# Kernel tuning notes

Measured on AMD Instinct MI355X. Metric: run time of the kernel, lower is better.

Reference implementation:

```python
import jax, jax.numpy as jnp
import numpy as np

EMBED_DIM = 512
Q_DIM = 64
V_DIM = 64
WINDOW_SIZE = 128
B, N = 2, 4096


def setup_inputs() -> dict:
    key = jax.random.key(0)
    ks = jax.random.split(key, 7)
    s = 1.0 / np.sqrt(EMBED_DIM)
    u = lambda k, shape: jax.random.uniform(k, shape, jnp.float32, -s, s)
    return {
        "x": jax.random.normal(ks[0], (B, N, EMBED_DIM), jnp.float32),
        "Wq": u(ks[1], (EMBED_DIM, Q_DIM)),
        "bq": u(ks[2], (Q_DIM,)),
        "Wk": u(ks[3], (EMBED_DIM, Q_DIM)),
        "bk": u(ks[4], (Q_DIM,)),
        "Wv": u(ks[5], (EMBED_DIM, V_DIM)),
        "bv": u(ks[6], (V_DIM,)),
    }


def reference(x, Wq, bq, Wk, bk, Wv, bv):
    b, n, _ = x.shape
    w = WINDOW_SIZE // 2
    Q = x @ Wq + bq  # (b, n, Qd)
    K = x @ Wk + bk  # (b, n, Qd)
    V = x @ Wv + bv  # (b, n, Vd)

    diags = jnp.arange(-w, w + 1)            # (nd,) offsets di
    nd = diags.shape[0]
    # Gather K[i + di] via padded K; invalid positions masked to 0 afterwards.
    Kpad = jnp.pad(K, ((0, 0), (w, w), (0, 0)))
    j = jnp.arange(n)[:, None] + diags[None, :]          # (n, nd) = i + di
    Kg = Kpad[:, j + w, :]                               # (b, n, nd, Qd)
    scores = jnp.einsum('bnd,bnod->bno', Q, Kg)          # (b, n, nd)
    valid = (j >= 0) & (j < n)
    scores = jnp.where(valid[None], scores, 0.0)

    # Faithful to original: diagonal dot products are scattered into the FIRST
    # nd columns of a dense (b, n, n) matrix (rest zeros), softmax over the
    # full n columns, then dense matmul with V.
    columns = jnp.zeros((b, n, n), dtype=x.dtype).at[:, :, :nd].set(scores)
    attn = jax.nn.softmax(columns, axis=2)               # (b, n, n)
    return attn @ V                                      # (b, n, Vd)
```

## Files before the change

### kernel.cpp

```cpp
#include <hip/hip_runtime.h>

typedef short short8 __attribute__((ext_vector_type(8)));
typedef float f32x4 __attribute__((ext_vector_type(4)));

#define NN 4096
#define NE 512
#define HD 64
#define KROWS 4288
#define KOFF  64

__device__ __forceinline__ unsigned short bf_trunc(float f) {
    union { float f; unsigned u; } c; c.f = f;
    return (unsigned short)(c.u >> 16);
}
__device__ __forceinline__ void bf_split(float f, unsigned short& hi, unsigned short& lo) {
    union { float f; unsigned u; } c; c.f = f;
    unsigned uh = c.u & 0xFFFF0000u;
    hi = (unsigned short)(uh >> 16);
    union { float f; unsigned u; } d; d.u = uh;
    lo = bf_trunc(f - d.f);
}

#define MFMA16(a, b, c) __builtin_amdgcn_mfma_f32_16x16x32_bf16((a), (b), (c), 0, 0, 0)

__global__ __launch_bounds__(256) void wprep_kernel(
    const float* __restrict__ Wq, const float* __restrict__ Wk,
    const float* __restrict__ Wv,
    unsigned short* __restrict__ Wfhi, unsigned short* __restrict__ Wflo,
    unsigned short* __restrict__ Khi, unsigned short* __restrict__ Klo,
    float* __restrict__ Vs)
{
    const int gtid = blockIdx.x * 256 + threadIdx.x;
    {
        const int L = gtid & 63;
        const int nt = (gtid >> 6) % 12;
        const int kt = gtid / 768;
        const int n = nt * 16 + (L & 15);
        const int kbase = kt * 32 + (L >> 4) * 8;
        const float* src; int col;
        if (n < 64)       { src = Wq; col = n; }
        else if (n < 128) { src = Wk; col = n - 64; }
        else              { src = Wv; col = n - 128; }
        short8 sh, sl;
#pragma unroll
        for (int j = 0; j < 8; ++j) {
            unsigned short h, l;
            bf_split(src[(size_t)(kbase + j) * HD + col], h, l);
            sh[j] = (short)h; sl[j] = (short)l;
        }
        *(short8*)(Wfhi + (size_t)gtid * 8) = sh;
        *(short8*)(Wflo + (size_t)gtid * 8) = sl;
    }
    if (gtid < 6144) {
        const int p = gtid >> 3, o = gtid & 7;
        const int b = p / 192, q = p - b * 192;
        const size_t row = (size_t)b * KROWS + (q < 64 ? q : 4096 + q);
        const short8 z = {0, 0, 0, 0, 0, 0, 0, 0};
        *(short8*)(Khi + row * HD + o * 8) = z;
        *(short8*)(Klo + row * HD + o * 8) = z;
    }
    if (gtid < 128) Vs[gtid] = 0.f;
}

__global__ __launch_bounds__(512) void proj_kernel(
    const float* __restrict__ x,
    const unsigned short* __restrict__ Wfhi, const unsigned short* __restrict__ Wflo,
    const float* __restrict__ bq, const float* __restrict__ bk,
    const float* __restrict__ bv,
    unsigned short* __restrict__ Qhi, unsigned short* __restrict__ Qlo,
    unsigned short* __restrict__ Khi, unsigned short* __restrict__ Klo,
    float* __restrict__ V129, float* __restrict__ Vs)
{
    __shared__ float vred[8][64];
    const int tid = threadIdx.x;
    const int L = tid & 63;
    const int w = tid >> 6;
    const int rt = w & 1, cg3 = w >> 1;
    const int m = L & 15, kg = L >> 4;
    const int r0 = blockIdx.x * 32;
    const int rowbase = r0 + rt * 16;

    const float* xp_base = x + (size_t)(rowbase + m) * NE + kg * 8;
    const unsigned short* wfh_base = Wfhi + (size_t)(cg3 * 3) * 512 + L * 8;
    const unsigned short* wfl_base = Wflo + (size_t)(cg3 * 3) * 512 + L * 8;

    f32x4 acc[3];
#pragma unroll
    for (int t = 0; t < 3; ++t) acc[t] = (f32x4){0.f, 0.f, 0.f, 0.f};

    float4 xa0 = *(const float4*)(xp_base);
    float4 xa1 = *(const float4*)(xp_base + 4);
    short8 wh0 = *(const short8*)(wfh_base + 0 * 512);
    short8 wh1 = *(const short8*)(wfh_base + 1 * 512);
    short8 wh2 = *(const short8*)(wfh_base + 2 * 512);
    short8 wl0 = *(const short8*)(wfl_base + 0 * 512);
    short8 wl1 = *(const short8*)(wfl_base + 1 * 512);
    short8 wl2 = *(const short8*)(wfl_base + 2 * 512);

    for (int kt = 0; kt < 16; ++kt) {
        const int ktn = (kt < 15) ? kt + 1 : 15;
        const float* xn = xp_base + ktn * 32;
        const float4 xb0 = *(const float4*)(xn);
        const float4 xb1 = *(const float4*)(xn + 4);
        const unsigned short* wnh = wfh_base + (size_t)ktn * 6144;
        const unsigned short* wnl = wfl_base + (size_t)ktn * 6144;
        const short8 nh0 = *(const short8*)(wnh);
        const short8 nh1 = *(const short8*)(wnh + 512);
        const short8 nh2 = *(const short8*)(wnh + 1024);
        const short8 nl0 = *(const short8*)(wnl);
        const short8 nl1 = *(const short8*)(wnl + 512);
        const short8 nl2 = *(const short8*)(wnl + 1024);

        const float xv[8] = {xa0.x, xa0.y, xa0.z, xa0.w,
                             xa1.x, xa1.y, xa1.z, xa1.w};
        short8 ahi, alo;
#pragma unroll
        for (int j = 0; j < 8; ++j) {
            unsigned short h, l; bf_split(xv[j], h, l);
            ahi[j] = (short)h; alo[j] = (short)l;
        }
        acc[0] = MFMA16(ahi, wh0, acc[0]);
        acc[0] = MFMA16(alo, wh0, acc[0]);
        acc[0] = MFMA16(ahi, wl0, acc[0]);
        acc[1] = MFMA16(ahi, wh1, acc[1]);
        acc[1] = MFMA16(alo, wh1, acc[1]);
        acc[1] = MFMA16(ahi, wl1, acc[1]);
        acc[2] = MFMA16(ahi, wh2, acc[2]);
        acc[2] = MFMA16(alo, wh2, acc[2]);
        acc[2] = MFMA16(ahi, wl2, acc[2]);

        xa0 = xb0; xa1 = xb1;
        wh0 = nh0; wh1 = nh1; wh2 = nh2;
        wl0 = nl0; wl1 = nl1; wl2 = nl2;
    }

    const int b = r0 >> 12;
#pragma unroll
    for (int t = 0; t < 3; ++t) {
        const int nt = cg3 * 3 + t;
        const int cg = nt * 16 + m;
        const float bias = (cg < 64) ? bq[cg] : (cg < 128) ? bk[cg - 64] : bv[cg - 128];
        float vsump = 0.f;
#pragma unroll
        for (int r = 0; r < 4; ++r) {
            const int gr = rowbase + kg * 4 + r;
            const float val = acc[t][r] + bias;
            if (cg < 64) {
                unsigned short h, l; bf_split(val, h, l);
                Qhi[(size_t)gr * HD + cg] = h;
                Qlo[(size_t)gr * HD + cg] = l;
            } else if (cg < 128) {
                const int d = cg - 64, n = gr & 4095;
                const size_t idx = ((size_t)b * KROWS + KOFF + n) * HD + d;
                unsigned short h, l; bf_split(val, h, l);
                Khi[idx] = h; Klo[idx] = l;
            } else {
                const int d = cg - 128, n = gr & 4095;
                vsump += val;
                if (n < 129) V129[((size_t)b * 129 + n) * HD + d] = val;
            }
        }
        if (cg >= 128) vred[rt * 4 + kg][cg - 128] = vsump;
    }
    __syncthreads();
    if (tid < 64) {
        float s = 0.f;
#pragma unroll
        for (int g = 0; g < 8; ++g) s += vred[g][tid];
        atomicAdd(&Vs[b * HD + tid], s);
    }
}

__global__ __launch_bounds__(256) void vprep_kernel(
    const float* __restrict__ V129,
    unsigned short* __restrict__ Vfhi, unsigned short* __restrict__ Vflo)
{
    const int tid = blockIdx.x * 256 + threadIdx.x;
    if (tid >= 3200) return;
    const int L = tid & 63;
    const int nt = (tid >> 6) % 5;
    const int jt = (tid / 320) % 5;
    const int b  = tid / 1600;
    const int n  = nt * 16 + (L & 15);
    const int jb = jt * 32 + (L >> 4) * 8;
    short8 sh, sl;
#pragma unroll
    for (int jj = 0; jj < 8; ++jj) {
        const int j = jb + jj;
        float val = 0.f;
        if (j < 129) {
            if (n < 64)       val = V129[((size_t)b * 129 + j) * HD + n];
            else if (n == 64) val = 1.0f;
        }
        unsigned short h, l; bf_split(val, h, l);
        sh[jj] = (short)h; sl[jj] = (short)l;
    }
    *(short8*)(Vfhi + (size_t)tid * 8) = sh;
    *(short8*)(Vflo + (size_t)tid * 8) = sl;
}

__global__ __launch_bounds__(256) void attn_kernel(
    const unsigned short* __restrict__ Qhi, const unsigned short* __restrict__ Qlo,
    const unsigned short* __restrict__ Khi, const unsigned short* __restrict__ Klo,
    const unsigned short* __restrict__ Vfhi, const unsigned short* __restrict__ Vflo,
    const float* __restrict__ Vs, float* __restrict__ out)
{
    __shared__ __align__(16) unsigned short wt_hi[16 * 168];
    __shared__ __align__(16) unsigned short wt_lo[16 * 168];
    __shared__ float den_lds[16];

    const int tid = threadIdx.x;
    const int L = tid & 63;
    const int w = tid >> 6;
    const int m = L & 15, kg = L >> 4;
    const int b = blockIdx.x >> 8;
    const int n0 = (blockIdx.x & 255) * 16;

    const unsigned short* qp  = Qhi + ((size_t)(b * NN + n0 + m)) * HD + kg * 8;
    const unsigned short* qp2 = Qlo + ((size_t)(b * NN + n0 + m)) * HD + kg * 8;
    const short8 qhi0 = *(const short8*)(qp);
    const short8 qhi1 = *(const short8*)(qp + 32);
    const short8 qlo0 = *(const short8*)(qp2);
    const short8 qlo1 = *(const short8*)(qp2 + 32);

    int kts[3]; int nkt;
    if (w == 3) { kts[0] = 3; kts[1] = 7; kts[2] = 8; nkt = 3; }
    else        { kts[0] = w; kts[1] = w + 4; kts[2] = 0; nkt = 2; }

    const unsigned short* KB  = Khi + (size_t)b * KROWS * HD;
    const unsigned short* KB2 = Klo + (size_t)b * KROWS * HD;
    short8 kh0[3], kh1[3], kl0[3], kl1[3];
#pragma unroll
    for (int i = 0; i < 3; ++i) {
        if (i < nkt) {
            const size_t krow = (size_t)(n0 + kts[i] * 16 + m);
            const unsigned short* kp  = KB  + krow * HD + kg * 8;
            const unsigned short* kp2 = KB2 + krow * HD + kg * 8;
            kh0[i] = *(const short8*)(kp);
            kh1[i] = *(const short8*)(kp + 32);
            kl0[i] = *(const short8*)(kp2);
            kl1[i] = *(const short8*)(kp2 + 32);
        }
    }

    short8 vhi[5], vlo[5], vh4[5];
#pragma unroll
    for (int jt = 0; jt < 5; ++jt) {
        const size_t fo = ((size_t)((b * 25 + jt * 5 + w) * 64 + L)) * 8;
        vhi[jt] = *(const short8*)(Vfhi + fo);
        vlo[jt] = *(const short8*)(Vflo + fo);
    }
    if (w == 0) {
#pragma unroll
        for (int jt = 0; jt < 5; ++jt) {
            const size_t fo4 = ((size_t)((b * 25 + jt * 5 + 4) * 64 + L)) * 8;
            vh4[jt] = *(const short8*)(Vfhi + fo4);
        }
    }

    for (int i = tid; i < (16 * 168) / 2; i += 256) {
        ((int*)wt_hi)[i] = 0;
        ((int*)wt_lo)[i] = 0;
    }
    __syncthreads();

#pragma unroll
    for (int i = 0; i < 3; ++i) {
        if (i < nkt) {
            f32x4 acc = (f32x4){0.f, 0.f, 0.f, 0.f};
            acc = MFMA16(qhi0, kh0[i], acc);
            acc = MFMA16(qhi1, kh1[i], acc);
            acc = MFMA16(qlo0, kh0[i], acc);
            acc = MFMA16(qlo1, kh1[i], acc);
            acc = MFMA16(qhi0, kl0[i], acc);
            acc = MFMA16(qhi1, kl1[i], acc);
            const int l = kts[i] * 16 + m;
#pragma unroll
            for (int r = 0; r < 4; ++r) {
                const int q = kg * 4 + r;
                const int j = l - q;
                if (j >= 0 && j < 129) {
                    const float wv = __expf(acc[r]) - 1.0f;
                    unsigned short h, lo2; bf_split(wv, h, lo2);
                    wt_hi[q * 168 + j] = h;
                    wt_lo[q * 168 + j] = lo2;
                }
            }
        }
    }
    __syncthreads();

    f32x4 oacc = (f32x4){0.f, 0.f, 0.f, 0.f};
    f32x4 dacc = (f32x4){0.f, 0.f, 0.f, 0.f};
#pragma unroll
    for (int jt = 0; jt < 5; ++jt) {
        const short8 whi = *(const short8*)(wt_hi + m * 168 + jt * 32 + kg * 8);
        const short8 wlo = *(const short8*)(wt_lo + m * 168 + jt * 32 + kg * 8);
        oacc = MFMA16(whi, vhi[jt], oacc);
        oacc = MFMA16(wlo, vhi[jt], oacc);
        oacc = MFMA16(whi, vlo[jt], oacc);
        if (w == 0) {
            dacc = MFMA16(whi, vh4[jt], dacc);
            dacc = MFMA16(wlo, vh4[jt], dacc);
        }
    }
    if (w == 0 && m == 0) {
#pragma unroll
        for (int r = 0; r < 4; ++r) den_lds[kg * 4 + r] = dacc[r];
    }
    __syncthreads();

    {
        const float vs = Vs[b * HD + w * 16 + m];
#pragma unroll
        for (int r = 0; r < 4; ++r) {
            const int q = kg * 4 + r;
            const float val = (vs + oacc[r]) / (4096.f + den_lds[q]);
            out[((size_t)(b * NN + n0 + q)) * HD + w * 16 + m] = val;
        }
    }
}

extern "C" void kernel_launch(void* const* d_in, const int* in_sizes, int n_in,
                              void* d_out, int out_size, void* d_ws, size_t ws_size,
                              hipStream_t stream)
{
    const float* x  = (const float*)d_in[0];
    const float* Wq = (const float*)d_in[1];
    const float* bq = (const float*)d_in[2];
    const float* Wk = (const float*)d_in[3];
    const float* bk = (const float*)d_in[4];
    const float* Wv = (const float*)d_in[5];
    const float* bv = (const float*)d_in[6];
    float* out = (float*)d_out;

    char* ws = (char*)d_ws;
    float*          Vs   = (float*)(ws + 0);
    unsigned short* Khi  = (unsigned short*)(ws + 512);
    unsigned short* Klo  = (unsigned short*)(ws + 1098240);
    unsigned short* Qhi  = (unsigned short*)(ws + 2195968);
    unsigned short* Qlo  = (unsigned short*)(ws + 3244544);
    float*          V129 = (float*)(ws + 4293120);
    unsigned short* Wfhi = (unsigned short*)(ws + 4359168);
    unsigned short* Wflo = (unsigned short*)(ws + 4555776);
    unsigned short* Vfhi = (unsigned short*)(ws + 4752384);
    unsigned short* Vflo = (unsigned short*)(ws + 4803584);

    wprep_kernel<<<48, 256, 0, stream>>>(Wq, Wk, Wv, Wfhi, Wflo, Khi, Klo, Vs);
    proj_kernel<<<256, 512, 0, stream>>>(x, Wfhi, Wflo, bq, bk, bv,
                                         Qhi, Qlo, Khi, Klo, V129, Vs);
    vprep_kernel<<<13, 256, 0, stream>>>(V129, Vfhi, Vflo);
    attn_kernel<<<512, 256, 0, stream>>>(Qhi, Qlo, Khi, Klo, Vfhi, Vflo, Vs, out);
}
```

Baseline: 102.3 us.

## Fuse four kernels into one cooperative kernel with grid-wide syncs

Replaces the four separate launches (weight prep, projection, V prep, attention) with a single cooperative kernel of 256 blocks of 512 threads, separated by grid.sync barriers. Each attention block now handles two 16-row query groups using two LDS buffers. The aim is to remove the per-launch overhead and the gaps between dependent kernels. In exchange it pays for three grid-wide barriers, depends on cooperative launch support, and limits the attention stage to 256 blocks.

Measured after the change: 185.1 us. 81.0% more time.

```diff
diff --git a/kernel.cpp b/kernel.cpp
--- a/kernel.cpp
+++ b/kernel.cpp
@@ -1,4 +1,7 @@
 #include <hip/hip_runtime.h>
+#include <hip/hip_cooperative_groups.h>
+
+namespace cg = cooperative_groups;
 
 typedef short short8 __attribute__((ext_vector_type(8)));
 typedef float f32x4 __attribute__((ext_vector_type(4)));
@@ -23,300 +26,300 @@
 
 #define MFMA16(a, b, c) __builtin_amdgcn_mfma_f32_16x16x32_bf16((a), (b), (c), 0, 0, 0)
 
-__global__ __launch_bounds__(256) void wprep_kernel(
-    const float* __restrict__ Wq, const float* __restrict__ Wk,
-    const float* __restrict__ Wv,
+__global__ __launch_bounds__(512) void fused_kernel(
+    const float* __restrict__ x,
+    const float* __restrict__ Wq, const float* __restrict__ bq,
+    const float* __restrict__ Wk, const float* __restrict__ bk,
+    const float* __restrict__ Wv, const float* __restrict__ bv,
     unsigned short* __restrict__ Wfhi, unsigned short* __restrict__ Wflo,
-    unsigned short* __restrict__ Khi, unsigned short* __restrict__ Klo,
-    float* __restrict__ Vs)
-{
-    const int gtid = blockIdx.x * 256 + threadIdx.x;
-    {
-        const int L = gtid & 63;
-        const int nt = (gtid >> 6) % 12;
-        const int kt = gtid / 768;
-        const int n = nt * 16 + (L & 15);
-        const int kbase = kt * 32 + (L >> 4) * 8;
-        const float* src; int col;
-        if (n < 64)       { src = Wq; col = n; }
-        else if (n < 128) { src = Wk; col = n - 64; }
-        else              { src = Wv; col = n - 128; }
-        short8 sh, sl;
-#pragma unroll
-        for (int j = 0; j < 8; ++j) {
-            unsigned short h, l;
-            bf_split(src[(size_t)(kbase + j) * HD + col], h, l);
-            sh[j] = (short)h; sl[j] = (short)l;
-        }
-        *(short8*)(Wfhi + (size_t)gtid * 8) = sh;
-        *(short8*)(Wflo + (size_t)gtid * 8) = sl;
-    }
-    if (gtid < 6144) {
-        const int p = gtid >> 3, o = gtid & 7;
-        const int b = p / 192, q = p - b * 192;
-        const size_t row = (size_t)b * KROWS + (q < 64 ? q : 4096 + q);
-        const short8 z = {0, 0, 0, 0, 0, 0, 0, 0};
-        *(short8*)(Khi + row * HD + o * 8) = z;
-        *(short8*)(Klo + row * HD + o * 8) = z;
-    }
-    if (gtid < 128) Vs[gtid] = 0.f;
-}
-
-__global__ __launch_bounds__(512) void proj_kernel(
-    const float* __restrict__ x,
-    const unsigned short* __restrict__ Wfhi, const unsigned short* __restrict__ Wflo,
-    const float* __restrict__ bq, const float* __restrict__ bk,
-    const float* __restrict__ bv,
     unsigned short* __restrict__ Qhi, unsigned short* __restrict__ Qlo,
     unsigned short* __restrict__ Khi, unsigned short* __restrict__ Klo,
-    float* __restrict__ V129, float* __restrict__ Vs)
+    float* __restrict__ V129,
+    unsigned short* __restrict__ Vfhi, unsigned short* __restrict__ Vflo,
+    float* __restrict__ Vs, float* __restrict__ out)
 {
-    __shared__ float vred[8][64];
-    const int tid = threadIdx.x;
-    const int L = tid & 63;
-    const int w = tid >> 6;
-    const int rt = w & 1, cg3 = w >> 1;
-    const int m = L & 15, kg = L >> 4;
-    const int r0 = blockIdx.x * 32;
-    const int rowbase = r0 + rt * 16;
-
-    const float* xp_base = x + (size_t)(rowbase + m) * NE + kg * 8;
-    const unsigned short* wfh_base = Wfhi + (size_t)(cg3 * 3) * 512 + L * 8;
-    const unsigned short* wfl_base = Wflo + (size_t)(cg3 * 3) * 512 + L * 8;
-
-    f32x4 acc[3];
-#pragma unroll
-    for (int t = 0; t < 3; ++t) acc[t] = (f32x4){0.f, 0.f, 0.f, 0.f};
-
-    float4 xa0 = *(const float4*)(xp_base);
-    float4 xa1 = *(const float4*)(xp_base + 4);
-    short8 wh0 = *(const short8*)(wfh_base + 0 * 512);
-    short8 wh1 = *(const short8*)(wfh_base + 1 * 512);
-    short8 wh2 = *(const short8*)(wfh_base + 2 * 512);
-    short8 wl0 = *(const short8*)(wfl_base + 0 * 512);
-    short8 wl1 = *(const short8*)(wfl_base + 1 * 512);
-    short8 wl2 = *(const short8*)(wfl_base + 2 * 512);
-
-    for (int kt = 0; kt < 16; ++kt) {
-        const int ktn = (kt < 15) ? kt + 1 : 15;
-        const float* xn = xp_base + ktn * 32;
-        const float4 xb0 = *(const float4*)(xn);
-        const float4 xb1 = *(const float4*)(xn + 4);
-        const unsigned short* wnh = wfh_base + (size_t)ktn * 6144;
-        const unsigned short* wnl = wfl_base + (size_t)ktn * 6144;
-        const short8 nh0 = *(const short8*)(wnh);
-        const short8 nh1 = *(const short8*)(wnh + 512);
-        const short8 nh2 = *(const short8*)(wnh + 1024);
-        const short8 nl0 = *(const short8*)(wnl);
-        const short8 nl1 = *(const short8*)(wnl + 512);
-        const short8 nl2 = *(const short8*)(wnl + 1024);
-
-        const float xv[8] = {xa0.x, xa0.y, xa0.z, xa0.w,
-                             xa1.x, xa1.y, xa1.z, xa1.w};
-        short8 ahi, alo;
-#pragma unroll
-        for (int j = 0; j < 8; ++j) {
-            unsigned short h, l; bf_split(xv[j], h, l);
-            ahi[j] = (short)h; alo[j] = (short)l;
-        }
-        acc[0] = MFMA16(ahi, wh0, acc[0]);
-        acc[0] = MFMA16(alo, wh0, acc[0]);
-        acc[0] = MFMA16(ahi, wl0, acc[0]);
-        acc[1] = MFMA16(ahi, wh1, acc[1]);
-        acc[1] = MFMA16(alo, wh1, acc[1]);
-        acc[1] = MFMA16(ahi, wl1, acc[1]);
-        acc[2] = MFMA16(ahi, wh2, acc[2]);
-        acc[2] = MFMA16(alo, wh2, acc[2]);
-        acc[2] = MFMA16(ahi, wl2, acc[2]);
-
-        xa0 = xb0; xa1 = xb1;
-        wh0 = nh0; wh1 = nh1; wh2 = nh2;
-        wl0 = nl0; wl1 = nl1; wl2 = nl2;
-    }
-
-    const int b = r0 >> 12;
-#pragma unroll
-    for (int t = 0; t < 3; ++t) {
-        const int nt = cg3 * 3 + t;
-        const int cg = nt * 16 + m;
-        const float bias = (cg < 64) ? bq[cg] : (cg < 128) ? bk[cg - 64] : bv[cg - 128];
-        float vsump = 0.f;
-#pragma unroll
-        for (int r = 0; r < 4; ++r) {
-            const int gr = rowbase + kg * 4 + r;
-            const float val = acc[t][r] + bias;
-            if (cg < 64) {
-                unsigned short h, l; bf_split(val, h, l);
-                Qhi[(size_t)gr * HD + cg] = h;
-                Qlo[(size_t)gr * HD + cg] = l;
-            } else if (cg < 128) {
-                const int d = cg - 64, n = gr & 4095;
-                const size_t idx = ((size_t)b * KROWS + KOFF + n) * HD + d;
-                unsigned short h, l; bf_split(val, h, l);
-                Khi[idx] = h; Klo[idx] = l;
-            } else {
-                const int d = cg - 128, n = gr & 4095;
-                vsump += val;
-                if (n < 129) V129[((size_t)b * 129 + n) * HD + d] = val;
-            }
-        }
-        if (cg >= 128) vred[rt * 4 + kg][cg - 128] = vsump;
-    }
-    __syncthreads();
-    if (tid < 64) {
-        float s = 0.f;
-#pragma unroll
-        for (int g = 0; g < 8; ++g) s += vred[g][tid];
-        atomicAdd(&Vs[b * HD + tid], s);
-    }
-}
-
-__global__ __launch_bounds__(256) void vprep_kernel(
-    const float* __restrict__ V129,
-    unsigned short* __restrict__ Vfhi, unsigned short* __restrict__ Vflo)
-{
-    const int tid = blockIdx.x * 256 + threadIdx.x;
-    if (tid >= 3200) return;
-    const int L = tid & 63;
-    const int nt = (tid >> 6) % 5;
-    const int jt = (tid / 320) % 5;
-    const int b  = tid / 1600;
-    const int n  = nt * 16 + (L & 15);
-    const int jb = jt * 32 + (L >> 4) * 8;
-    short8 sh, sl;
-#pragma unroll
-    for (int jj = 0; jj < 8; ++jj) {
-        const int j = jb + jj;
-        float val = 0.f;
-        if (j < 129) {
-            if (n < 64)       val = V129[((size_t)b * 129 + j) * HD + n];
-            else if (n == 64) val = 1.0f;
-        }
-        unsigned short h, l; bf_split(val, h, l);
-        sh[jj] = (short)h; sl[jj] = (short)l;
-    }
-    *(short8*)(Vfhi + (size_t)tid * 8) = sh;
-    *(short8*)(Vflo + (size_t)tid * 8) = sl;
-}
-
-__global__ __launch_bounds__(256) void attn_kernel(
-    const unsigned short* __restrict__ Qhi, const unsigned short* __restrict__ Qlo,
-    const unsigned short* __restrict__ Khi, const unsigned short* __restrict__ Klo,
-    const unsigned short* __restrict__ Vfhi, const unsigned short* __restrict__ Vflo,
-    const float* __restrict__ Vs, float* __restrict__ out)
-{
-    __shared__ __align__(16) unsigned short wt_hi[16 * 168];
-    __shared__ __align__(16) unsigned short wt_lo[16 * 168];
-    __shared__ float den_lds[16];
-
+    cg::grid_group grid = cg::this_grid();
+    const int blk = blockIdx.x;
     const int tid = threadIdx.x;
     const int L = tid & 63;
     const int w = tid >> 6;
     const int m = L & 15, kg = L >> 4;
-    const int b = blockIdx.x >> 8;
-    const int n0 = (blockIdx.x & 255) * 16;
-
-    const unsigned short* qp  = Qhi + ((size_t)(b * NN + n0 + m)) * HD + kg * 8;
-    const unsigned short* qp2 = Qlo + ((size_t)(b * NN + n0 + m)) * HD + kg * 8;
-    const short8 qhi0 = *(const short8*)(qp);
-    const short8 qhi1 = *(const short8*)(qp + 32);
-    const short8 qlo0 = *(const short8*)(qp2);
-    const short8 qlo1 = *(const short8*)(qp2 + 32);
-
-    int kts[3]; int nkt;
-    if (w == 3) { kts[0] = 3; kts[1] = 7; kts[2] = 8; nkt = 3; }
-    else        { kts[0] = w; kts[1] = w + 4; kts[2] = 0; nkt = 2; }
-
-    const unsigned short* KB  = Khi + (size_t)b * KROWS * HD;
-    const unsigned short* KB2 = Klo + (size_t)b * KROWS * HD;
-    short8 kh0[3], kh1[3], kl0[3], kl1[3];
-#pragma unroll
-    for (int i = 0; i < 3; ++i) {
-        if (i < nkt) {
-            const size_t krow = (size_t)(n0 + kts[i] * 16 + m);
-            const unsigned short* kp  = KB  + krow * HD + kg * 8;
-            const unsigned short* kp2 = KB2 + krow * HD + kg * 8;
-            kh0[i] = *(const short8*)(kp);
-            kh1[i] = *(const short8*)(kp + 32);
-            kl0[i] = *(const short8*)(kp2);
-            kl1[i] = *(const short8*)(kp2 + 32);
-        }
+
+    __shared__ float vred[8][64];
+    __shared__ __align__(16) unsigned short wt_hi[2][16 * 168];
+    __shared__ __align__(16) unsigned short wt_lo[2][16 * 168];
+    __shared__ float den_lds[2][16];
+
+    {
+        const int gtid = blk * 512 + tid;
+        if (gtid < 12288) {
+            const int nt = (gtid >> 6) % 12;
+            const int kt = gtid / 768;
+            const int n = nt * 16 + m;
+            const int kbase = kt * 32 + kg * 8;
+            const float* src; int col;
+            if (n < 64)       { src = Wq; col = n; }
+            else if (n < 128) { src = Wk; col = n - 64; }
+            else              { src = Wv; col = n - 128; }
+            short8 sh, sl;
+#pragma unroll
+            for (int j = 0; j < 8; ++j) {
+                unsigned short h, l;
+                bf_split(src[(size_t)(kbase + j) * HD + col], h, l);
+                sh[j] = (short)h; sl[j] = (short)l;
+            }
+            *(short8*)(Wfhi + (size_t)gtid * 8) = sh;
+            *(short8*)(Wflo + (size_t)gtid * 8) = sl;
+        }
+        if (gtid < 6144) {
+            const int p = gtid >> 3, o = gtid & 7;
+            const int b = p / 192, q = p - b * 192;
+            const size_t row = (size_t)b * KROWS + (q < 64 ? q : 4096 + q);
+            const short8 z = {0, 0, 0, 0, 0, 0, 0, 0};
+            *(short8*)(Khi + row * HD + o * 8) = z;
+            *(short8*)(Klo + row * HD + o * 8) = z;
+        }
+        if (gtid < 128) Vs[gtid] = 0.f;
     }
-
-    short8 vhi[5], vlo[5], vh4[5];
-#pragma unroll
-    for (int jt = 0; jt < 5; ++jt) {
-        const size_t fo = ((size_t)((b * 25 + jt * 5 + w) * 64 + L)) * 8;
-        vhi[jt] = *(const short8*)(Vfhi + fo);
-        vlo[jt] = *(const short8*)(Vflo + fo);
+    grid.sync();
+
+    {
+        const int rt = w & 1, cg3 = w >> 1;
+        const int r0 = blk * 32;
+        const int rowbase = r0 + rt * 16;
+
+        const float* xp_base = x + (size_t)(rowbase + m) * NE + kg * 8;
+        const unsigned short* wfh_base = Wfhi + (size_t)(cg3 * 3) * 512 + L * 8;
+        const unsigned short* wfl_base = Wflo + (size_t)(cg3 * 3) * 512 + L * 8;
+
+        f32x4 acc[3];
+#pragma unroll
+        for (int t = 0; t < 3; ++t) acc[t] = (f32x4){0.f, 0.f, 0.f, 0.f};
+
+        float4 xa0 = *(const float4*)(xp_base);
+        float4 xa1 = *(const float4*)(xp_base + 4);
+        short8 wh0 = *(const short8*)(wfh_base + 0 * 512);
+        short8 wh1 = *(const short8*)(wfh_base + 1 * 512);
+        short8 wh2 = *(const short8*)(wfh_base + 2 * 512);
+        short8 wl0 = *(const short8*)(wfl_base + 0 * 512);
+        short8 wl1 = *(const short8*)(wfl_base + 1 * 512);
+        short8 wl2 = *(const short8*)(wfl_base + 2 * 512);
+
+#pragma unroll 2
+        for (int kt = 0; kt < 16; ++kt) {
+            const int ktn = (kt < 15) ? kt + 1 : 15;
+            const float* xn = xp_base + ktn * 32;
+            const float4 xb0 = *(const float4*)(xn);
+            const float4 xb1 = *(const float4*)(xn + 4);
+            const unsigned short* wnh = wfh_base + (size_t)ktn * 6144;
+            const unsigned short* wnl = wfl_base + (size_t)ktn * 6144;
+            const short8 nh0 = *(const short8*)(wnh);
+            const short8 nh1 = *(const short8*)(wnh + 512);
+            const short8 nh2 = *(const short8*)(wnh + 1024);
+            const short8 nl0 = *(const short8*)(wnl);
+            const short8 nl1 = *(const short8*)(wnl + 512);
+            const short8 nl2 = *(const short8*)(wnl + 1024);
+
+            const float xv[8] = {xa0.x, xa0.y, xa0.z, xa0.w,
+                                 xa1.x, xa1.y, xa1.z, xa1.w};
+            short8 ahi, alo;
+#pragma unroll
+            for (int j = 0; j < 8; ++j) {
+                unsigned short h, l; bf_split(xv[j], h, l);
+                ahi[j] = (short)h; alo[j] = (short)l;
+            }
+            acc[0] = MFMA16(ahi, wh0, acc[0]);
+            acc[0] = MFMA16(alo, wh0, acc[0]);
+            acc[0] = MFMA16(ahi, wl0, acc[0]);
+            acc[1] = MFMA16(ahi, wh1, acc[1]);
+            acc[1] = MFMA16(alo, wh1, acc[1]);
+            acc[1] = MFMA16(ahi, wl1, acc[1]);
+            acc[2] = MFMA16(ahi, wh2, acc[2]);
+            acc[2] = MFMA16(alo, wh2, acc[2]);
+            acc[2] = MFMA16(ahi, wl2, acc[2]);
+
+            xa0 = xb0; xa1 = xb1;
+            wh0 = nh0; wh1 = nh1; wh2 = nh2;
+            wl0 = nl0; wl1 = nl1; wl2 = nl2;
+        }
+
+        const int b = r0 >> 12;
+#pragma unroll
+        for (int t = 0; t < 3; ++t) {
+            const int nt = cg3 * 3 + t;
+            const int cgc = nt * 16 + m;
+            const float bias = (cgc < 64) ? bq[cgc]
+                             : (cgc < 128) ? bk[cgc - 64] : bv[cgc - 128];
+            float vsump = 0.f;
+#pragma unroll
+            for (int r = 0; r < 4; ++r) {
+                const int gr = rowbase + kg * 4 + r;
+                const float val = acc[t][r] + bias;
+                if (cgc < 64) {
+                    unsigned short h, l; bf_split(val, h, l);
+                    Qhi[(size_t)gr * HD + cgc] = h;
+                    Qlo[(size_t)gr * HD + cgc] = l;
+                } else if (cgc < 128) {
+                    const int d = cgc - 64, n = gr & 4095;
+                    const size_t idx = ((size_t)b * KROWS + KOFF + n) * HD + d;
+                    unsigned short h, l; bf_split(val, h, l);
+                    Khi[idx] = h; Klo[idx] = l;
+                } else {
+                    const int d = cgc - 128, n = gr & 4095;
+                    vsump += val;
+                    if (n < 129) V129[((size_t)b * 129 + n) * HD + d] = val;
+                }
+            }
+            if (cgc >= 128) vred[rt * 4 + kg][cgc - 128] = vsump;
+        }
+        __syncthreads();
+        if (tid < 64) {
+            float s = 0.f;
+#pragma unroll
+            for (int g = 0; g < 8; ++g) s += vred[g][tid];
+            atomicAdd(&Vs[b * HD + tid], s);
+        }
     }
-    if (w == 0) {
+    grid.sync();
+
+    {
+        const int gtid = blk * 512 + tid;
+        if (gtid < 3200) {
+            const int nt = (gtid >> 6) % 5;
+            const int jt = (gtid / 320) % 5;
+            const int b  = gtid / 1600;
+            const int n  = nt * 16 + m;
+            const int jb = jt * 32 + kg * 8;
+            short8 sh, sl;
+#pragma unroll
+            for (int jj = 0; jj < 8; ++jj) {
+                const int j = jb + jj;
+                float val = 0.f;
+                if (j < 129) {
+                    if (n < 64)       val = V129[((size_t)b * 129 + j) * HD + n];
+                    else if (n == 64) val = 1.0f;
+                }
+                unsigned short h, l; bf_split(val, h, l);
+                sh[jj] = (short)h; sl[jj] = (short)l;
+            }
+            *(short8*)(Vfhi + (size_t)gtid * 8) = sh;
+            *(short8*)(Vflo + (size_t)gtid * 8) = sl;
+        }
+    }
+    grid.sync();
+
+    {
+        const int g  = w >> 2;
+        const int wv = w & 3;
+        const int vblk = blk * 2 + g;
+        const int b  = vblk >> 8;
+        const int n0 = (vblk & 255) * 16;
+
+        const unsigned short* qp  = Qhi + ((size_t)(b * NN + n0 + m)) * HD + kg * 8;
+        const unsigned short* qp2 = Qlo + ((size_t)(b * NN + n0 + m)) * HD + kg * 8;
+        const short8 qhi0 = *(const short8*)(qp);
+        const short8 qhi1 = *(const short8*)(qp + 32);
+        const short8 qlo0 = *(const short8*)(qp2);
+        const short8 qlo1 = *(const short8*)(qp2 + 32);
+
+        int kts[3]; int nkt;
+        if (wv == 3) { kts[0] = 3; kts[1] = 7; kts[2] = 8; nkt = 3; }
+        else         { kts[0] = wv; kts[1] = wv + 4; kts[2] = 0; nkt = 2; }
+
+        const unsigned short* KB  = Khi + (size_t)b * KROWS * HD;
+        const unsigned short* KB2 = Klo + (size_t)b * KROWS * HD;
+        short8 kh0[3], kh1[3], kl0[3], kl1[3];
+#pragma unroll
+        for (int i = 0; i < 3; ++i) {
+            if (i < nkt) {
+                const size_t krow = (size_t)(n0 + kts[i] * 16 + m);
+                const unsigned short* kp  = KB  + krow * HD + kg * 8;
+                const unsigned short* kp2 = KB2 + krow * HD + kg * 8;
+                kh0[i] = *(const short8*)(kp);
+                kh1[i] = *(const short8*)(kp + 32);
+                kl0[i] = *(const short8*)(kp2);
+                kl1[i] = *(const short8*)(kp2 + 32);
+            }
+        }
+
+        short8 vhi[5], vlo[5], vh4[5];
 #pragma unroll
         for (int jt = 0; jt < 5; ++jt) {
-            const size_t fo4 = ((size_t)((b * 25 + jt * 5 + 4) * 64 + L)) * 8;
-            vh4[jt] = *(const short8*)(Vfhi + fo4);
-        }
-    }
-
-    for (int i = tid; i < (16 * 168) / 2; i += 256) {
-        ((int*)wt_hi)[i] = 0;
-        ((int*)wt_lo)[i] = 0;
-    }
-    __syncthreads();
-
-#pragma unroll
-    for (int i = 0; i < 3; ++i) {
-        if (i < nkt) {
-            f32x4 acc = (f32x4){0.f, 0.f, 0.f, 0.f};
-            acc = MFMA16(qhi0, kh0[i], acc);
-            acc = MFMA16(qhi1, kh1[i], acc);
-            acc = MFMA16(qlo0, kh0[i], acc);
-            acc = MFMA16(qlo1, kh1[i], acc);
-            acc = MFMA16(qhi0, kl0[i], acc);
-            acc = MFMA16(qhi1, kl1[i], acc);
-            const int l = kts[i] * 16 + m;
+            const size_t fo = ((size_t)((b * 25 + jt * 5 + wv) * 64 + L)) * 8;
+            vhi[jt] = *(const short8*)(Vfhi + fo);
+            vlo[jt] = *(const short8*)(Vflo + fo);
+        }
+        if (wv == 0) {
+#pragma unroll
+            for (int jt = 0; jt < 5; ++jt) {
+                const size_t fo4 = ((size_t)((b * 25 + jt * 5 + 4) * 64 + L)) * 8;
+                vh4[jt] = *(const short8*)(Vfhi + fo4);
+            }
+        }
+
+        {
+            const int lt = (wv << 6) | L;
+            for (int i = lt; i < (16 * 168) / 2; i += 256) {
+                ((int*)wt_hi[g])[i] = 0;
+                ((int*)wt_lo[g])[i] = 0;
+            }
+        }
+        __syncthreads();
+
+#pragma unroll
+        for (int i = 0; i < 3; ++i) {
+            if (i < nkt) {
+                f32x4 acc = (f32x4){0.f, 0.f, 0.f, 0.f};
+                acc = MFMA16(qhi0, kh0[i], acc);
+                acc = MFMA16(qhi1, kh1[i], acc);
+                acc = MFMA16(qlo0, kh0[i], acc);
+                acc = MFMA16(qlo1, kh1[i], acc);
+                acc = MFMA16(qhi0, kl0[i], acc);
+                acc = MFMA16(qhi1, kl1[i], acc);
+                const int l = kts[i] * 16 + m;
+#pragma unroll
+                for (int r = 0; r < 4; ++r) {
+                    const int q = kg * 4 + r;
+                    const int j = l - q;
+                    if (j >= 0 && j < 129) {
+                        const float wval = __expf(acc[r]) - 1.0f;
+                        unsigned short h, lo2; bf_split(wval, h, lo2);
+                        wt_hi[g][q * 168 + j] = h;
+                        wt_lo[g][q * 168 + j] = lo2;
+                    }
+                }
+            }
+        }
+        __syncthreads();
+
+        f32x4 oacc = (f32x4){0.f, 0.f, 0.f, 0.f};
+        f32x4 dacc = (f32x4){0.f, 0.f, 0.f, 0.f};
+#pragma unroll
+        for (int jt = 0; jt < 5; ++jt) {
+            const short8 whi = *(const short8*)(wt_hi[g] + m * 168 + jt * 32 + kg * 8);
+            const short8 wlo = *(const short8*)(wt_lo[g] + m * 168 + jt * 32 + kg * 8);
+            oacc = MFMA16(whi, vhi[jt], oacc);
+            oacc = MFMA16(wlo, vhi[jt], oacc);
+            oacc = MFMA16(whi, vlo[jt], oacc);
+            if (wv == 0) {
+                dacc = MFMA16(whi, vh4[jt], dacc);
+                dacc = MFMA16(wlo, vh4[jt], dacc);
+            }
+        }
+        if (wv == 0 && m == 0) {
+#pragma unroll
+            for (int r = 0; r < 4; ++r) den_lds[g][kg * 4 + r] = dacc[r];
+        }
+        __syncthreads();
+
+        {
+            const float vs = Vs[b * HD + wv * 16 + m];
 #pragma unroll
             for (int r = 0; r < 4; ++r) {
                 const int q = kg * 4 + r;
-                const int j = l - q;
-                if (j >= 0 && j < 129) {
-                    const float wv = __expf(acc[r]) - 1.0f;
-                    unsigned short h, lo2; bf_split(wv, h, lo2);
-                    wt_hi[q * 168 + j] = h;
-                    wt_lo[q * 168 + j] = lo2;
-                }
-            }
-        }
-    }
-    __syncthreads();
-
-    f32x4 oacc = (f32x4){0.f, 0.f, 0.f, 0.f};
-    f32x4 dacc = (f32x4){0.f, 0.f, 0.f, 0.f};
-#pragma unroll
-    for (int jt = 0; jt < 5; ++jt) {
-        const short8 whi = *(const short8*)(wt_hi + m * 168 + jt * 32 + kg * 8);
-        const short8 wlo = *(const short8*)(wt_lo + m * 168 + jt * 32 + kg * 8);
-        oacc = MFMA16(whi, vhi[jt], oacc);
-        oacc = MFMA16(wlo, vhi[jt], oacc);
-        oacc = MFMA16(whi, vlo[jt], oacc);
-        if (w == 0) {
-            dacc = MFMA16(whi, vh4[jt], dacc);
-            dacc = MFMA16(wlo, vh4[jt], dacc);
-        }
-    }
-    if (w == 0 && m == 0) {
-#pragma unroll
-        for (int r = 0; r < 4; ++r) den_lds[kg * 4 + r] = dacc[r];
-    }
-    __syncthreads();
-
-    {
-        const float vs = Vs[b * HD + w * 16 + m];
-#pragma unroll
-        for (int r = 0; r < 4; ++r) {
-            const int q = kg * 4 + r;
-            const float val = (vs + oacc[r]) / (4096.f + den_lds[q]);
-            out[((size_t)(b * NN + n0 + q)) * HD + w * 16 + m] = val;
+                const float val = (vs + oacc[r]) / (4096.f + den_lds[g][q]);
+                out[((size_t)(b * NN + n0 + q)) * HD + wv * 16 + m] = val;
+            }
         }
     }
 }
@@ -346,9 +349,14 @@
     unsigned short* Vfhi = (unsigned short*)(ws + 4752384);
     unsigned short* Vflo = (unsigned short*)(ws + 4803584);
 
-    wprep_kernel<<<48, 256, 0, stream>>>(Wq, Wk, Wv, Wfhi, Wflo, Khi, Klo, Vs);
-    proj_kernel<<<256, 512, 0, stream>>>(x, Wfhi, Wflo, bq, bk, bv,
-                                         Qhi, Qlo, Khi, Klo, V129, Vs);
-    vprep_kernel<<<13, 256, 0, stream>>>(V129, Vfhi, Vflo);
-    attn_kernel<<<512, 256, 0, stream>>>(Qhi, Qlo, Khi, Klo, Vfhi, Vflo, Vs, out);
+    void* kargs[] = {
+        (void*)&x, (void*)&Wq, (void*)&bq, (void*)&Wk, (void*)&bk,
+        (void*)&Wv, (void*)&bv,
+        (void*)&Wfhi, (void*)&Wflo,
+        (void*)&Qhi, (void*)&Qlo, (void*)&Khi, (void*)&Klo,
+        (void*)&V129, (void*)&Vfhi, (void*)&Vflo,
+        (void*)&Vs, (void*)&out
+    };
+    hipLaunchCooperativeKernel(fused_kernel, dim3(256), dim3(512),
+                               kargs, 0, stream);
 }
```

## Fold V fragment prep into projection kernel and deepen load pipeline

Applied to the files above, without the earlier changes.

Removes the separate vprep kernel and its V129 intermediate. The projection kernel now writes the bf16 hi/lo V fragments straight from a shared-memory tile of V, and wprep pre-fills the constant ones-column and zero padding. The projection kernel moves to 16-row blocks of 256 threads (512 blocks, two per CU via launch bounds) with a three-stage register prefetch of x and weights. The aim is one fewer launch and no global round trip for V, at the cost of more registers for the deeper prefetch.

Result: slower. 104.6 us (+2.2%).

```diff
diff --git a/kernel.cpp b/kernel.cpp
--- a/kernel.cpp
+++ b/kernel.cpp
@@ -28,11 +28,12 @@
     const float* __restrict__ Wv,
     unsigned short* __restrict__ Wfhi, unsigned short* __restrict__ Wflo,
     unsigned short* __restrict__ Khi, unsigned short* __restrict__ Klo,
+    unsigned short* __restrict__ Vfhi, unsigned short* __restrict__ Vflo,
     float* __restrict__ Vs)
 {
     const int gtid = blockIdx.x * 256 + threadIdx.x;
+    const int L = gtid & 63;
     {
-        const int L = gtid & 63;
         const int nt = (gtid >> 6) % 12;
         const int kt = gtid / 768;
         const int n = nt * 16 + (L & 15);
@@ -59,144 +60,148 @@
         *(short8*)(Khi + row * HD + o * 8) = z;
         *(short8*)(Klo + row * HD + o * 8) = z;
     }
+    if (gtid < 3200) {
+        const int rem = gtid % 1600;
+        const int jt = rem / 320;
+        const int nt = (rem / 64) % 5;
+        short8 sh = {0, 0, 0, 0, 0, 0, 0, 0};
+        const short8 z = {0, 0, 0, 0, 0, 0, 0, 0};
+        if (nt == 4 && (L & 15) == 0) {
+#pragma unroll
+            for (int jj = 0; jj < 8; ++jj) {
+                const int j = jt * 32 + (L >> 4) * 8 + jj;
+                if (j < 129) sh[jj] = (short)0x3F80;
+            }
+        }
+        *(short8*)(Vfhi + (size_t)gtid * 8) = sh;
+        *(short8*)(Vflo + (size_t)gtid * 8) = z;
+    }
     if (gtid < 128) Vs[gtid] = 0.f;
 }
 
-__global__ __launch_bounds__(512) void proj_kernel(
+__global__ __launch_bounds__(256, 2) void proj_kernel(
     const float* __restrict__ x,
     const unsigned short* __restrict__ Wfhi, const unsigned short* __restrict__ Wflo,
     const float* __restrict__ bq, const float* __restrict__ bk,
     const float* __restrict__ bv,
     unsigned short* __restrict__ Qhi, unsigned short* __restrict__ Qlo,
     unsigned short* __restrict__ Khi, unsigned short* __restrict__ Klo,
-    float* __restrict__ V129, float* __restrict__ Vs)
+    unsigned short* __restrict__ Vfhi, unsigned short* __restrict__ Vflo,
+    float* __restrict__ Vs)
 {
-    __shared__ float vred[8][64];
+    __shared__ float V_lds[16][68];
     const int tid = threadIdx.x;
     const int L = tid & 63;
     const int w = tid >> 6;
-    const int rt = w & 1, cg3 = w >> 1;
     const int m = L & 15, kg = L >> 4;
-    const int r0 = blockIdx.x * 32;
-    const int rowbase = r0 + rt * 16;
-
-    const float* xp_base = x + (size_t)(rowbase + m) * NE + kg * 8;
-    const unsigned short* wfh_base = Wfhi + (size_t)(cg3 * 3) * 512 + L * 8;
-    const unsigned short* wfl_base = Wflo + (size_t)(cg3 * 3) * 512 + L * 8;
+    const int blk = blockIdx.x;
+    const int r0 = blk * 16;
+    const int b = blk >> 8;
+
+    const float* xp = x + (size_t)(r0 + m) * NE + kg * 8;
+    const unsigned short* wfh = Wfhi + (size_t)(w * 3) * 512 + L * 8;
+    const unsigned short* wfl = Wflo + (size_t)(w * 3) * 512 + L * 8;
 
     f32x4 acc[3];
 #pragma unroll
     for (int t = 0; t < 3; ++t) acc[t] = (f32x4){0.f, 0.f, 0.f, 0.f};
 
-    float4 xa0 = *(const float4*)(xp_base);
-    float4 xa1 = *(const float4*)(xp_base + 4);
-    short8 wh0 = *(const short8*)(wfh_base + 0 * 512);
-    short8 wh1 = *(const short8*)(wfh_base + 1 * 512);
-    short8 wh2 = *(const short8*)(wfh_base + 2 * 512);
-    short8 wl0 = *(const short8*)(wfl_base + 0 * 512);
-    short8 wl1 = *(const short8*)(wfl_base + 1 * 512);
-    short8 wl2 = *(const short8*)(wfl_base + 2 * 512);
-
+    float4 cx0[3], cx1[3];
+    short8 cwh[3][3], cwl[3][3];
+
+#pragma unroll
+    for (int p = 0; p < 2; ++p) {
+        cx0[p] = *(const float4*)(xp + p * 32);
+        cx1[p] = *(const float4*)(xp + p * 32 + 4);
+#pragma unroll
+        for (int t = 0; t < 3; ++t) {
+            cwh[p][t] = *(const short8*)(wfh + (size_t)p * 6144 + t * 512);
+            cwl[p][t] = *(const short8*)(wfl + (size_t)p * 6144 + t * 512);
+        }
+    }
+
+#pragma unroll
     for (int kt = 0; kt < 16; ++kt) {
-        const int ktn = (kt < 15) ? kt + 1 : 15;
-        const float* xn = xp_base + ktn * 32;
-        const float4 xb0 = *(const float4*)(xn);
-        const float4 xb1 = *(const float4*)(xn + 4);
-        const unsigned short* wnh = wfh_base + (size_t)ktn * 6144;
-        const unsigned short* wnl = wfl_base + (size_t)ktn * 6144;
-        const short8 nh0 = *(const short8*)(wnh);
-        const short8 nh1 = *(const short8*)(wnh + 512);
-        const short8 nh2 = *(const short8*)(wnh + 1024);
-        const short8 nl0 = *(const short8*)(wnl);
-        const short8 nl1 = *(const short8*)(wnl + 512);
-        const short8 nl2 = *(const short8*)(wnl + 1024);
-
-        const float xv[8] = {xa0.x, xa0.y, xa0.z, xa0.w,
-                             xa1.x, xa1.y, xa1.z, xa1.w};
+        const int cur = kt % 3;
+        const int nxt = (kt + 2) % 3;
+        if (kt + 2 < 16) {
+            cx0[nxt] = *(const float4*)(xp + (kt + 2) * 32);
+            cx1[nxt] = *(const float4*)(xp + (kt + 2) * 32 + 4);
+#pragma unroll
+            for (int t = 0; t < 3; ++t) {
+                cwh[nxt][t] = *(const short8*)(wfh + (size_t)(kt + 2) * 6144 + t * 512);
+                cwl[nxt][t] = *(const short8*)(wfl + (size_t)(kt + 2) * 6144 + t * 512);
+            }
+        }
+        const float xv[8] = {cx0[cur].x, cx0[cur].y, cx0[cur].z, cx0[cur].w,
+                             cx1[cur].x, cx1[cur].y, cx1[cur].z, cx1[cur].w};
         short8 ahi, alo;
 #pragma unroll
         for (int j = 0; j < 8; ++j) {
             unsigned short h, l; bf_split(xv[j], h, l);
             ahi[j] = (short)h; alo[j] = (short)l;
         }
-        acc[0] = MFMA16(ahi, wh0, acc[0]);
-        acc[0] = MFMA16(alo, wh0, acc[0]);
-        acc[0] = MFMA16(ahi, wl0, acc[0]);
-        acc[1] = MFMA16(ahi, wh1, acc[1]);
-        acc[1] = MFMA16(alo, wh1, acc[1]);
-        acc[1] = MFMA16(ahi, wl1, acc[1]);
-        acc[2] = MFMA16(ahi, wh2, acc[2]);
-        acc[2] = MFMA16(alo, wh2, acc[2]);
-        acc[2] = MFMA16(ahi, wl2, acc[2]);
-
-        xa0 = xb0; xa1 = xb1;
-        wh0 = nh0; wh1 = nh1; wh2 = nh2;
-        wl0 = nl0; wl1 = nl1; wl2 = nl2;
-    }
-
-    const int b = r0 >> 12;
+#pragma unroll
+        for (int t = 0; t < 3; ++t) {
+            acc[t] = MFMA16(ahi, cwh[cur][t], acc[t]);
+            acc[t] = MFMA16(alo, cwh[cur][t], acc[t]);
+            acc[t] = MFMA16(ahi, cwl[cur][t], acc[t]);
+        }
+    }
+
 #pragma unroll
     for (int t = 0; t < 3; ++t) {
-        const int nt = cg3 * 3 + t;
-        const int cg = nt * 16 + m;
-        const float bias = (cg < 64) ? bq[cg] : (cg < 128) ? bk[cg - 64] : bv[cg - 128];
-        float vsump = 0.f;
+        const int nt = w * 3 + t;
+        const int cgc = nt * 16 + m;
+        const float bias = (cgc < 64) ? bq[cgc]
+                         : (cgc < 128) ? bk[cgc - 64] : bv[cgc - 128];
 #pragma unroll
         for (int r = 0; r < 4; ++r) {
-            const int gr = rowbase + kg * 4 + r;
+            const int gr = r0 + kg * 4 + r;
             const float val = acc[t][r] + bias;
-            if (cg < 64) {
+            if (cgc < 64) {
                 unsigned short h, l; bf_split(val, h, l);
-                Qhi[(size_t)gr * HD + cg] = h;
-                Qlo[(size_t)gr * HD + cg] = l;
-            } else if (cg < 128) {
-                const int d = cg - 64, n = gr & 4095;
+                Qhi[(size_t)gr * HD + cgc] = h;
+                Qlo[(size_t)gr * HD + cgc] = l;
+            } else if (cgc < 128) {
+                const int d = cgc - 64, n = gr & 4095;
                 const size_t idx = ((size_t)b * KROWS + KOFF + n) * HD + d;
                 unsigned short h, l; bf_split(val, h, l);
                 Khi[idx] = h; Klo[idx] = l;
             } else {
-                const int d = cg - 128, n = gr & 4095;
-                vsump += val;
-                if (n < 129) V129[((size_t)b * 129 + n) * HD + d] = val;
-            }
-        }
-        if (cg >= 128) vred[rt * 4 + kg][cg - 128] = vsump;
+                V_lds[kg * 4 + r][cgc - 128] = val;
+            }
+        }
     }
     __syncthreads();
+
     if (tid < 64) {
         float s = 0.f;
 #pragma unroll
-        for (int g = 0; g < 8; ++g) s += vred[g][tid];
+        for (int r = 0; r < 16; ++r) s += V_lds[r][tid];
         atomicAdd(&Vs[b * HD + tid], s);
     }
-}
-
-__global__ __launch_bounds__(256) void vprep_kernel(
-    const float* __restrict__ V129,
-    unsigned short* __restrict__ Vfhi, unsigned short* __restrict__ Vflo)
-{
-    const int tid = blockIdx.x * 256 + threadIdx.x;
-    if (tid >= 3200) return;
-    const int L = tid & 63;
-    const int nt = (tid >> 6) % 5;
-    const int jt = (tid / 320) % 5;
-    const int b  = tid / 1600;
-    const int n  = nt * 16 + (L & 15);
-    const int jb = jt * 32 + (L >> 4) * 8;
-    short8 sh, sl;
-#pragma unroll
-    for (int jj = 0; jj < 8; ++jj) {
-        const int j = jb + jj;
-        float val = 0.f;
-        if (j < 129) {
-            if (n < 64)       val = V129[((size_t)b * 129 + j) * HD + n];
-            else if (n == 64) val = 1.0f;
-        }
-        unsigned short h, l; bf_split(val, h, l);
-        sh[jj] = (short)h; sl[jj] = (short)l;
-    }
-    *(short8*)(Vfhi + (size_t)tid * 8) = sh;
-    *(short8*)(Vflo + (size_t)tid * 8) = sl;
+
+    if ((blk & 255) <= 8) {
+        const int n0v = r0 & 4095;
+        const int jt = n0v >> 5;
+        const int h = (n0v >> 4) & 1;
+        if ((kg >> 1) == h) {
+            const int nt = w;
+            short8 sh, sl;
+#pragma unroll
+            for (int jj = 0; jj < 8; ++jj) {
+                const int j = jt * 32 + kg * 8 + jj;
+                float val = 0.f;
+                if (j < 129) val = V_lds[j - n0v][nt * 16 + m];
+                unsigned short hh, ll; bf_split(val, hh, ll);
+                sh[jj] = (short)hh; sl[jj] = (short)ll;
+            }
+            const size_t fo = ((size_t)((b * 25 + jt * 5 + nt) * 64 + L)) * 8;
+            *(short8*)(Vfhi + fo) = sh;
+            *(short8*)(Vflo + fo) = sl;
+        }
+    }
 }
 
 __global__ __launch_bounds__(256) void attn_kernel(
@@ -280,8 +285,8 @@
                 const int q = kg * 4 + r;
                 const int j = l - q;
                 if (j >= 0 && j < 129) {
-                    const float wv = __expf(acc[r]) - 1.0f;
-                    unsigned short h, lo2; bf_split(wv, h, lo2);
+                    const float wval = __expf(acc[r]) - 1.0f;
+                    unsigned short h, lo2; bf_split(wval, h, lo2);
                     wt_hi[q * 168 + j] = h;
                     wt_lo[q * 168 + j] = lo2;
                 }
@@ -340,15 +345,14 @@
     unsigned short* Klo  = (unsigned short*)(ws + 1098240);
     unsigned short* Qhi  = (unsigned short*)(ws + 2195968);
     unsigned short* Qlo  = (unsigned short*)(ws + 3244544);
-    float*          V129 = (float*)(ws + 4293120);
     unsigned short* Wfhi = (unsigned short*)(ws + 4359168);
     unsigned short* Wflo = (unsigned short*)(ws + 4555776);
     unsigned short* Vfhi = (unsigned short*)(ws + 4752384);
     unsigned short* Vflo = (unsigned short*)(ws + 4803584);
 
-    wprep_kernel<<<48, 256, 0, stream>>>(Wq, Wk, Wv, Wfhi, Wflo, Khi, Klo, Vs);
-    proj_kernel<<<256, 512, 0, stream>>>(x, Wfhi, Wflo, bq, bk, bv,
-                                         Qhi, Qlo, Khi, Klo, V129, Vs);
-    vprep_kernel<<<13, 256, 0, stream>>>(V129, Vfhi, Vflo);
+    wprep_kernel<<<48, 256, 0, stream>>>(Wq, Wk, Wv, Wfhi, Wflo,
+                                         Khi, Klo, Vfhi, Vflo, Vs);
+    proj_kernel<<<512, 256, 0, stream>>>(x, Wfhi, Wflo, bq, bk, bv,
+                                         Qhi, Qlo, Khi, Klo, Vfhi, Vflo, Vs);
     attn_kernel<<<512, 256, 0, stream>>>(Qhi, Qlo, Khi, Klo, Vfhi, Vflo, Vs, out);
 }
```
